# Kernel tuning notes

Hardware: AMD Instinct MI355X
Metric: run time of the kernel (lower is better)

Reference implementation:

```python
import jax, jax.numpy as jnp
import numpy as np

KERNEL_MUL = 2.0
KERNEL_NUM = 5


def setup_inputs() -> dict:
    key = jax.random.key(0)
    k1, k2 = jax.random.split(key)
    N, D = 4096, 512
    source = jax.random.normal(k1, (N, D), dtype=jnp.float32)
    target = jax.random.normal(k2, (N, D), dtype=jnp.float32)
    return {"source": source, "target": target}


def _mmd(source, target):
    n = source.shape[0]
    total = jnp.concatenate([source, target], axis=0)  # [2N, D]
    # pairwise squared L2 via the ||a||^2 + ||b||^2 - 2 a.b identity (same math,
    # avoids materializing the [2N,2N,D] expanded tensor the torch code builds)
    sq = jnp.sum(total * total, axis=1)  # [2N]
    L2 = sq[:, None] + sq[None, :] - 2.0 * (total @ total.T)  # [2N, 2N]
    m = total.shape[0]
    # torch uses L2_distance.data -> detached bandwidth
    bandwidth = jax.lax.stop_gradient(jnp.sum(L2)) / (m * m - m)
    bandwidth = bandwidth / (KERNEL_MUL ** (KERNEL_NUM // 2))
    kernels = jnp.zeros_like(L2)
    for i in range(KERNEL_NUM):
        kernels = kernels + jnp.exp(-L2 / (bandwidth * (KERNEL_MUL ** i)))
    XX = kernels[:n, :n]
    YY = kernels[n:, n:]
    XY = kernels[:n, n:]
    YX = kernels[n:, :n]
    return jnp.mean(XX + YY - XY - YX)


def reference(source, target):
    return _mmd(source, target)
```

## Files before the change

### kernel.cpp

```cpp
#include <hip/hip_runtime.h>
#include <hip/hip_fp8.h>

#define NHALF 4096
#define NROWS 8192
#define D 512
#define BM 128
#define BKB 128
#define NKT (D / BKB)
#define NB (NROWS / BM)
#define NTRI (NB * (NB + 1) / 2)

typedef float f32x4 __attribute__((ext_vector_type(4)));

__device__ __forceinline__ const float* row_ptr(const float* __restrict__ src,
                                                const float* __restrict__ tgt, int r) {
    return (r < NHALF) ? (src + (size_t)r * D) : (tgt + (size_t)(r - NHALF) * D);
}

__global__ __launch_bounds__(256)
void conv_stats(const float* __restrict__ src, const float* __restrict__ tgt,
                unsigned char* __restrict__ tot8, float* __restrict__ sq,
                float* __restrict__ colsum, double* __restrict__ sumsq) {
    __shared__ float cs_lds[4][512];
    int t = threadIdx.x, l = t & 63, w = t >> 6;
    int rbase = blockIdx.x * 64 + w * 16;

    float cs[8] = {0.f, 0.f, 0.f, 0.f, 0.f, 0.f, 0.f, 0.f};
    float ssq = 0.f;

    for (int rr = 0; rr < 16; ++rr) {
        int r = rbase + rr;
        const float* p = row_ptr(src, tgt, r) + l * 8;
        float4 v0 = *(const float4*)p;
        float4 v1 = *(const float4*)(p + 4);
        union { unsigned long long u; unsigned char b[8]; } q;
        q.b[0] = __hip_fp8_e4m3(v0.x).__x; q.b[1] = __hip_fp8_e4m3(v0.y).__x;
        q.b[2] = __hip_fp8_e4m3(v0.z).__x; q.b[3] = __hip_fp8_e4m3(v0.w).__x;
        q.b[4] = __hip_fp8_e4m3(v1.x).__x; q.b[5] = __hip_fp8_e4m3(v1.y).__x;
        q.b[6] = __hip_fp8_e4m3(v1.z).__x; q.b[7] = __hip_fp8_e4m3(v1.w).__x;
        unsigned dstu = (unsigned)((l & 48) | ((l & 15) ^ (r & 15)));
        *(unsigned long long*)&tot8[(size_t)r * D + dstu * 8] = q.u;

        float s8 = v0.x*v0.x + v0.y*v0.y + v0.z*v0.z + v0.w*v0.w
                 + v1.x*v1.x + v1.y*v1.y + v1.z*v1.z + v1.w*v1.w;
        ssq += s8;
        cs[0] += v0.x; cs[1] += v0.y; cs[2] += v0.z; cs[3] += v0.w;
        cs[4] += v1.x; cs[5] += v1.y; cs[6] += v1.z; cs[7] += v1.w;
        float rsum = s8;
        for (int off = 32; off > 0; off >>= 1) rsum += __shfl_down(rsum, off);
        if (l == 0) sq[r] = rsum;
    }
#pragma unroll
    for (int j = 0; j < 8; ++j) cs_lds[w][l * 8 + j] = cs[j];
    for (int off = 32; off > 0; off >>= 1) ssq += __shfl_down(ssq, off);
    __shared__ float wssq[4];
    if (l == 0) wssq[w] = ssq;
    __syncthreads();
    int c0 = t * 2;
    float a = cs_lds[0][c0] + cs_lds[1][c0] + cs_lds[2][c0] + cs_lds[3][c0];
    float b = cs_lds[0][c0+1] + cs_lds[1][c0+1] + cs_lds[2][c0+1] + cs_lds[3][c0+1];
    atomicAdd(&colsum[c0], a);
    atomicAdd(&colsum[c0 + 1], b);
    if (t == 0) atomicAdd(sumsq, (double)(wssq[0] + wssq[1] + wssq[2] + wssq[3]));
}

__global__ void bw_kernel(const float* __restrict__ colsum, const double* __restrict__ sumsq,
                          float* __restrict__ inv16bw) {
    __shared__ double red[512];
    int c = threadIdx.x;
    double v = (double)colsum[c];
    red[c] = v * v;
    __syncthreads();
    for (int s = 256; s > 0; s >>= 1) {
        if (c < s) red[c] += red[c + s];
        __syncthreads();
    }
    if (c == 0) {
        double m = (double)NROWS;
        double sumL2 = 2.0 * m * sumsq[0] - 2.0 * red[0];
        double bw = sumL2 / (m * m - m);
        bw = bw / 4.0;
        inv16bw[0] = (float)(1.0 / (16.0 * bw));
    }
}

__global__ __launch_bounds__(256)
void mmd_main(const unsigned char* __restrict__ tot8,
              const float* __restrict__ sq, const float* __restrict__ inv16bw_p,
              double* __restrict__ S) {
    int b = blockIdx.x;
    int ti = (b & 7) * (NTRI / 8) + (b >> 3);
    int bi = (int)(64.5f - sqrtf(64.5f * 64.5f - 2.0f * (float)ti));
    if (bi < 0) bi = 0;
    while (bi > 0 && bi * NB - bi * (bi - 1) / 2 > ti) --bi;
    while ((bi + 1) * NB - (bi + 1) * bi / 2 <= ti) ++bi;
    int bj = bi + (ti - (bi * NB - bi * (bi - 1) / 2));

    __shared__ __align__(16) unsigned char As[BM * BKB];
    __shared__ __align__(16) unsigned char Bs[BM * BKB];

    int t = threadIdx.x, l = t & 63, w = t >> 6;
    int wr = w >> 1, wc = w & 1;
    int m = l & 15, kg = l >> 4;

    const unsigned char* ab = tot8 + (size_t)(bi * BM) * D;
    const unsigned char* bb = tot8 + (size_t)(bj * BM) * D;

    f32x4 acc[4][4];
#pragma unroll
    for (int i = 0; i < 4; ++i)
#pragma unroll
        for (int j = 0; j < 4; ++j)
            acc[i][j] = (f32x4){0.f, 0.f, 0.f, 0.f};

    for (int kt = 0; kt < NKT; ++kt) {
        __syncthreads();
#pragma unroll
        for (int i = 0; i < 4; ++i) {
            int g = i * 256 + t;
            int row = g >> 3, ch = g & 7;
            __builtin_amdgcn_global_load_lds(
                (const __attribute__((address_space(1))) void*)(ab + (size_t)row * D + kt * BKB + ch * 16),
                (__attribute__((address_space(3))) void*)(As + g * 16),
                16, 0, 0);
            __builtin_amdgcn_global_load_lds(
                (const __attribute__((address_space(1))) void*)(bb + (size_t)row * D + kt * BKB + ch * 16),
                (__attribute__((address_space(3))) void*)(Bs + g * 16),
                16, 0, 0);
        }
        __syncthreads();

#pragma unroll
        for (int ks = 0; ks < 4; ++ks) {
            long af[4], bfr[4];
#pragma unroll
            for (int fi = 0; fi < 4; ++fi) {
                int row = wr * 64 + fi * 16 + m;
                int unit = (ks * 4 + kg) ^ m;
                af[fi] = *(const long*)&As[row * BKB + unit * 8];
            }
#pragma unroll
            for (int fj = 0; fj < 4; ++fj) {
                int row = wc * 64 + fj * 16 + m;
                int unit = (ks * 4 + kg) ^ m;
                bfr[fj] = *(const long*)&Bs[row * BKB + unit * 8];
            }
#pragma unroll
            for (int fi = 0; fi < 4; ++fi)
#pragma unroll
                for (int fj = 0; fj < 4; ++fj)
                    acc[fi][fj] = __builtin_amdgcn_mfma_f32_16x16x32_fp8_fp8(af[fi], bfr[fj], acc[fi][fj], 0, 0, 0);
        }
    }

    float inv16bw = inv16bw_p[0];
    float coef = ((bi == bj) ? 1.f : 2.f) * (((bi < NB / 2) == (bj < NB / 2)) ? 1.f : -1.f);

    float sqj[4];
#pragma unroll
    for (int fj = 0; fj < 4; ++fj) sqj[fj] = sq[bj * BM + wc * 64 + fj * 16 + m];
    int ib = bi * BM + wr * 64 + kg * 4;

    float local = 0.f;
#pragma unroll
    for (int fi = 0; fi < 4; ++fi) {
        float sqi[4];
#pragma unroll
        for (int j = 0; j < 4; ++j) sqi[j] = sq[ib + fi * 16 + j];
#pragma unroll
        for (int fj = 0; fj < 4; ++fj) {
#pragma unroll
            for (int j = 0; j < 4; ++j) {
                float L2 = sqi[j] + sqj[fj] - 2.f * acc[fi][fj][j];
                float u = __expf(-L2 * inv16bw);
                float ks = u;
                u *= u; ks += u;
                u *= u; ks += u;
                u *= u; ks += u;
                u *= u; ks += u;
                if (bi == bj) {
                    int ig = wr * 64 + fi * 16 + kg * 4 + j;
                    int jg = wc * 64 + fj * 16 + m;
                    if (ig == jg) ks = 5.0f;
                }
                local += ks;
            }
        }
    }
    local *= coef;

    for (int off = 32; off > 0; off >>= 1) local += __shfl_down(local, off);
    __shared__ float wsum[4];
    if ((t & 63) == 0) wsum[t >> 6] = local;
    __syncthreads();
    if (t == 0) {
        float bsum = wsum[0] + wsum[1] + wsum[2] + wsum[3];
        atomicAdd(S, (double)bsum);
    }
}

__global__ void finalize_kernel(const double* __restrict__ S, float* __restrict__ out) {
    out[0] = (float)(S[0] / ((double)NHALF * (double)NHALF));
}

extern "C" void kernel_launch(void* const* d_in, const int* in_sizes, int n_in,
                              void* d_out, int out_size, void* d_ws, size_t ws_size,
                              hipStream_t stream) {
    const float* src = (const float*)d_in[0];
    const float* tgt = (const float*)d_in[1];
    float* out = (float*)d_out;
    char* ws = (char*)d_ws;

    unsigned char* tot8 = (unsigned char*)ws;
    float*  sq      = (float*)(ws + 4194304);
    float*  colsum  = (float*)(ws + 4194304 + 32768);
    double* sumsq   = (double*)(ws + 4194304 + 34816);
    double* S       = (double*)(ws + 4194304 + 34824);
    float*  inv16bw = (float*)(ws + 4194304 + 34832);

    hipMemsetAsync(ws + 4194304 + 32768, 0, 2068, stream);

    conv_stats<<<128, 256, 0, stream>>>(src, tgt, tot8, sq, colsum, sumsq);
    bw_kernel<<<1, 512, 0, stream>>>(colsum, sumsq, inv16bw);
    mmd_main<<<NTRI, 256, 0, stream>>>(tot8, sq, inv16bw, S);
    finalize_kernel<<<1, 1, 0, stream>>>(S, out);
}
```

Before: 73.73 us.

## Use scaled 16x16x128 fp8 MFMA, fold bandwidth calc into main kernel

Replaces four 16x16x32 fp8 MFMAs per fragment with one gfx950 scaled 16x16x128 f8f6f4 MFMA, using unit scales. This cuts the MFMA instruction count, and the LDS fragment reads are regrouped per k-tile. The separate bandwidth kernel is removed: every main block recomputes inv16bw from colsum while its first tile loads, which saves a launch but repeats a small reduction in each block (in float instead of double). conv_stats also gets twice as many blocks with half the rows each, and mmd_main gets a launch-bounds occupancy hint of 3.

```diff
diff --git a/kernel.cpp b/kernel.cpp
--- a/kernel.cpp
+++ b/kernel.cpp
@@ -11,6 +11,7 @@
 #define NTRI (NB * (NB + 1) / 2)
 
 typedef float f32x4 __attribute__((ext_vector_type(4)));
+typedef int   v8i   __attribute__((ext_vector_type(8)));
 
 __device__ __forceinline__ const float* row_ptr(const float* __restrict__ src,
                                                 const float* __restrict__ tgt, int r) {
@@ -23,12 +24,12 @@
                 float* __restrict__ colsum, double* __restrict__ sumsq) {
     __shared__ float cs_lds[4][512];
     int t = threadIdx.x, l = t & 63, w = t >> 6;
-    int rbase = blockIdx.x * 64 + w * 16;
+    int rbase = blockIdx.x * 32 + w * 8;
 
     float cs[8] = {0.f, 0.f, 0.f, 0.f, 0.f, 0.f, 0.f, 0.f};
     float ssq = 0.f;
 
-    for (int rr = 0; rr < 16; ++rr) {
+    for (int rr = 0; rr < 8; ++rr) {
         int r = rbase + rr;
         const float* p = row_ptr(src, tgt, r) + l * 8;
         float4 v0 = *(const float4*)p;
@@ -64,30 +65,10 @@
     if (t == 0) atomicAdd(sumsq, (double)(wssq[0] + wssq[1] + wssq[2] + wssq[3]));
 }
 
-__global__ void bw_kernel(const float* __restrict__ colsum, const double* __restrict__ sumsq,
-                          float* __restrict__ inv16bw) {
-    __shared__ double red[512];
-    int c = threadIdx.x;
-    double v = (double)colsum[c];
-    red[c] = v * v;
-    __syncthreads();
-    for (int s = 256; s > 0; s >>= 1) {
-        if (c < s) red[c] += red[c + s];
-        __syncthreads();
-    }
-    if (c == 0) {
-        double m = (double)NROWS;
-        double sumL2 = 2.0 * m * sumsq[0] - 2.0 * red[0];
-        double bw = sumL2 / (m * m - m);
-        bw = bw / 4.0;
-        inv16bw[0] = (float)(1.0 / (16.0 * bw));
-    }
-}
-
-__global__ __launch_bounds__(256)
+__global__ __launch_bounds__(256, 3)
 void mmd_main(const unsigned char* __restrict__ tot8,
-              const float* __restrict__ sq, const float* __restrict__ inv16bw_p,
-              double* __restrict__ S) {
+              const float* __restrict__ sq, const float* __restrict__ colsum,
+              const double* __restrict__ sumsq, double* __restrict__ S) {
     int b = blockIdx.x;
     int ti = (b & 7) * (NTRI / 8) + (b >> 3);
     int bi = (int)(64.5f - sqrtf(64.5f * 64.5f - 2.0f * (float)ti));
@@ -106,15 +87,7 @@
     const unsigned char* ab = tot8 + (size_t)(bi * BM) * D;
     const unsigned char* bb = tot8 + (size_t)(bj * BM) * D;
 
-    f32x4 acc[4][4];
-#pragma unroll
-    for (int i = 0; i < 4; ++i)
-#pragma unroll
-        for (int j = 0; j < 4; ++j)
-            acc[i][j] = (f32x4){0.f, 0.f, 0.f, 0.f};
-
-    for (int kt = 0; kt < NKT; ++kt) {
-        __syncthreads();
+    auto stage = [&](int kt) {
 #pragma unroll
         for (int i = 0; i < 4; ++i) {
             int g = i * 256 + t;
@@ -128,32 +101,65 @@
                 (__attribute__((address_space(3))) void*)(Bs + g * 16),
                 16, 0, 0);
         }
-        __syncthreads();
-
-#pragma unroll
-        for (int ks = 0; ks < 4; ++ks) {
-            long af[4], bfr[4];
-#pragma unroll
-            for (int fi = 0; fi < 4; ++fi) {
-                int row = wr * 64 + fi * 16 + m;
-                int unit = (ks * 4 + kg) ^ m;
-                af[fi] = *(const long*)&As[row * BKB + unit * 8];
+    };
+
+    stage(0);
+
+    float c1 = colsum[t], c2 = colsum[t + 256];
+    float part = c1 * c1 + c2 * c2;
+    for (int off = 32; off > 0; off >>= 1) part += __shfl_down(part, off);
+    __shared__ float bwl[4];
+    if (l == 0) bwl[w] = part;
+    __syncthreads();
+    float sumcol2 = bwl[0] + bwl[1] + bwl[2] + bwl[3];
+    double md = (double)NROWS;
+    double sumL2 = 2.0 * md * sumsq[0] - 2.0 * (double)sumcol2;
+    double bwv = sumL2 / (md * md - md) / 4.0;
+    float inv16bw = (float)(1.0 / (16.0 * bwv));
+
+    f32x4 acc[4][4];
+#pragma unroll
+    for (int i = 0; i < 4; ++i)
+#pragma unroll
+        for (int j = 0; j < 4; ++j)
+            acc[i][j] = (f32x4){0.f, 0.f, 0.f, 0.f};
+
+    __syncthreads();
+
+    for (int kt = 0; kt < NKT; ++kt) {
+        union Frag { v8i v; long q[4]; };
+        Frag fa[4];
+#pragma unroll
+        for (int fi = 0; fi < 4; ++fi) {
+            int row = wr * 64 + fi * 16 + m;
+#pragma unroll
+            for (int q = 0; q < 4; ++q) {
+                int unit = (q * 4 + kg) ^ m;
+                fa[fi].q[q] = *(const long*)&As[row * BKB + unit * 8];
             }
-#pragma unroll
-            for (int fj = 0; fj < 4; ++fj) {
-                int row = wc * 64 + fj * 16 + m;
-                int unit = (ks * 4 + kg) ^ m;
-                bfr[fj] = *(const long*)&Bs[row * BKB + unit * 8];
+        }
+#pragma unroll
+        for (int fj = 0; fj < 4; ++fj) {
+            Frag fb;
+            int row = wc * 64 + fj * 16 + m;
+#pragma unroll
+            for (int q = 0; q < 4; ++q) {
+                int unit = (q * 4 + kg) ^ m;
+                fb.q[q] = *(const long*)&Bs[row * BKB + unit * 8];
             }
 #pragma unroll
             for (int fi = 0; fi < 4; ++fi)
-#pragma unroll
-                for (int fj = 0; fj < 4; ++fj)
-                    acc[fi][fj] = __builtin_amdgcn_mfma_f32_16x16x32_fp8_fp8(af[fi], bfr[fj], acc[fi][fj], 0, 0, 0);
-        }
-    }
-
-    float inv16bw = inv16bw_p[0];
+                acc[fi][fj] = __builtin_amdgcn_mfma_scale_f32_16x16x128_f8f6f4(
+                    fa[fi].v, fb.v, acc[fi][fj], 0, 0,
+                    0, 0x7F7F7F7F, 0, 0x7F7F7F7F);
+        }
+        if (kt + 1 < NKT) {
+            __syncthreads();
+            stage(kt + 1);
+            __syncthreads();
+        }
+    }
+
     float coef = ((bi == bj) ? 1.f : 2.f) * (((bi < NB / 2) == (bj < NB / 2)) ? 1.f : -1.f);
 
     float sqj[4];
@@ -216,12 +222,10 @@
     float*  colsum  = (float*)(ws + 4194304 + 32768);
     double* sumsq   = (double*)(ws + 4194304 + 34816);
     double* S       = (double*)(ws + 4194304 + 34824);
-    float*  inv16bw = (float*)(ws + 4194304 + 34832);
-
-    hipMemsetAsync(ws + 4194304 + 32768, 0, 2068, stream);
-
-    conv_stats<<<128, 256, 0, stream>>>(src, tgt, tot8, sq, colsum, sumsq);
-    bw_kernel<<<1, 512, 0, stream>>>(colsum, sumsq, inv16bw);
-    mmd_main<<<NTRI, 256, 0, stream>>>(tot8, sq, inv16bw, S);
+
+    hipMemsetAsync(ws + 4194304 + 32768, 0, 2064, stream);
+
+    conv_stats<<<256, 256, 0, stream>>>(src, tgt, tot8, sq, colsum, sumsq);
+    mmd_main<<<NTRI, 256, 0, stream>>>(tot8, sq, colsum, sumsq, S);
     finalize_kernel<<<1, 1, 0, stream>>>(S, out);
 }
```

Result: no change. 73.13 us (-0.8%).

## Fuse bandwidth reduction into conv kernel and use 8-wave GEMM blocks

Applied to the files above, without the earlier changes.

The separate bandwidth kernel is folded into conv_stats: the last block to finish, found with an atomic ticket, reduces the column sums and writes the inverse bandwidth, which removes one kernel launch. conv_stats now uses twice as many blocks with half the rows each. mmd_main moves to 512 threads and 8 waves per 128x128 tile, so each wave computes a 64x32 sub-tile, giving fewer accumulator registers and more waves to hide latency. The trade is more per-tile syncs and fewer MFMAs per wave between them, and the memset still covers the ticket, so the fused path stays correct.

```diff
diff --git a/kernel.cpp b/kernel.cpp
--- a/kernel.cpp
+++ b/kernel.cpp
@@ -9,6 +9,7 @@
 #define NKT (D / BKB)
 #define NB (NROWS / BM)
 #define NTRI (NB * (NB + 1) / 2)
+#define CONV_BLOCKS 256
 
 typedef float f32x4 __attribute__((ext_vector_type(4)));
 
@@ -20,15 +21,19 @@
 __global__ __launch_bounds__(256)
 void conv_stats(const float* __restrict__ src, const float* __restrict__ tgt,
                 unsigned char* __restrict__ tot8, float* __restrict__ sq,
-                float* __restrict__ colsum, double* __restrict__ sumsq) {
+                float* __restrict__ colsum, double* __restrict__ sumsq,
+                unsigned* __restrict__ ticket, float* __restrict__ inv16bw_out) {
     __shared__ float cs_lds[4][512];
+    __shared__ float wssq[4];
+    __shared__ int lastFlag;
+    __shared__ double red[256];
     int t = threadIdx.x, l = t & 63, w = t >> 6;
-    int rbase = blockIdx.x * 64 + w * 16;
+    int rbase = blockIdx.x * 32 + w * 8;
 
     float cs[8] = {0.f, 0.f, 0.f, 0.f, 0.f, 0.f, 0.f, 0.f};
     float ssq = 0.f;
 
-    for (int rr = 0; rr < 16; ++rr) {
+    for (int rr = 0; rr < 8; ++rr) {
         int r = rbase + rr;
         const float* p = row_ptr(src, tgt, r) + l * 8;
         float4 v0 = *(const float4*)p;
@@ -53,7 +58,6 @@
 #pragma unroll
     for (int j = 0; j < 8; ++j) cs_lds[w][l * 8 + j] = cs[j];
     for (int off = 32; off > 0; off >>= 1) ssq += __shfl_down(ssq, off);
-    __shared__ float wssq[4];
     if (l == 0) wssq[w] = ssq;
     __syncthreads();
     int c0 = t * 2;
@@ -62,29 +66,34 @@
     atomicAdd(&colsum[c0], a);
     atomicAdd(&colsum[c0 + 1], b);
     if (t == 0) atomicAdd(sumsq, (double)(wssq[0] + wssq[1] + wssq[2] + wssq[3]));
-}
-
-__global__ void bw_kernel(const float* __restrict__ colsum, const double* __restrict__ sumsq,
-                          float* __restrict__ inv16bw) {
-    __shared__ double red[512];
-    int c = threadIdx.x;
-    double v = (double)colsum[c];
-    red[c] = v * v;
-    __syncthreads();
-    for (int s = 256; s > 0; s >>= 1) {
-        if (c < s) red[c] += red[c + s];
+    __syncthreads();
+
+    if (t == 0) {
+        __threadfence();
+        unsigned old = atomicAdd(ticket, 1u);
+        lastFlag = (old == CONV_BLOCKS - 1) ? 1 : 0;
+    }
+    __syncthreads();
+    if (lastFlag) {
+        float ca = atomicAdd(&colsum[t], 0.f);
+        float cb = atomicAdd(&colsum[t + 256], 0.f);
+        red[t] = (double)ca * ca + (double)cb * cb;
         __syncthreads();
-    }
-    if (c == 0) {
-        double m = (double)NROWS;
-        double sumL2 = 2.0 * m * sumsq[0] - 2.0 * red[0];
-        double bw = sumL2 / (m * m - m);
-        bw = bw / 4.0;
-        inv16bw[0] = (float)(1.0 / (16.0 * bw));
-    }
-}
-
-__global__ __launch_bounds__(256)
+        for (int s = 128; s > 0; s >>= 1) {
+            if (t < s) red[t] += red[t + s];
+            __syncthreads();
+        }
+        if (t == 0) {
+            double ssqd = atomicAdd(sumsq, 0.0);
+            double m = (double)NROWS;
+            double sumL2 = 2.0 * m * ssqd - 2.0 * red[0];
+            double bw = sumL2 / (m * m - m) / 4.0;
+            inv16bw_out[0] = (float)(1.0 / (16.0 * bw));
+        }
+    }
+}
+
+__global__ __launch_bounds__(512, 4)
 void mmd_main(const unsigned char* __restrict__ tot8,
               const float* __restrict__ sq, const float* __restrict__ inv16bw_p,
               double* __restrict__ S) {
@@ -100,24 +109,24 @@
     __shared__ __align__(16) unsigned char Bs[BM * BKB];
 
     int t = threadIdx.x, l = t & 63, w = t >> 6;
-    int wr = w >> 1, wc = w & 1;
+    int wr = w >> 2, wc = w & 3;
     int m = l & 15, kg = l >> 4;
 
     const unsigned char* ab = tot8 + (size_t)(bi * BM) * D;
     const unsigned char* bb = tot8 + (size_t)(bj * BM) * D;
 
-    f32x4 acc[4][4];
+    f32x4 acc[4][2];
 #pragma unroll
     for (int i = 0; i < 4; ++i)
 #pragma unroll
-        for (int j = 0; j < 4; ++j)
+        for (int j = 0; j < 2; ++j)
             acc[i][j] = (f32x4){0.f, 0.f, 0.f, 0.f};
 
     for (int kt = 0; kt < NKT; ++kt) {
         __syncthreads();
 #pragma unroll
-        for (int i = 0; i < 4; ++i) {
-            int g = i * 256 + t;
+        for (int i = 0; i < 2; ++i) {
+            int g = i * 512 + t;
             int row = g >> 3, ch = g & 7;
             __builtin_amdgcn_global_load_lds(
                 (const __attribute__((address_space(1))) void*)(ab + (size_t)row * D + kt * BKB + ch * 16),
@@ -132,7 +141,7 @@
 
 #pragma unroll
         for (int ks = 0; ks < 4; ++ks) {
-            long af[4], bfr[4];
+            long af[4], bfr[2];
 #pragma unroll
             for (int fi = 0; fi < 4; ++fi) {
                 int row = wr * 64 + fi * 16 + m;
@@ -140,15 +149,15 @@
                 af[fi] = *(const long*)&As[row * BKB + unit * 8];
             }
 #pragma unroll
-            for (int fj = 0; fj < 4; ++fj) {
-                int row = wc * 64 + fj * 16 + m;
+            for (int fj = 0; fj < 2; ++fj) {
+                int row = wc * 32 + fj * 16 + m;
                 int unit = (ks * 4 + kg) ^ m;
                 bfr[fj] = *(const long*)&Bs[row * BKB + unit * 8];
             }
 #pragma unroll
             for (int fi = 0; fi < 4; ++fi)
 #pragma unroll
-                for (int fj = 0; fj < 4; ++fj)
+                for (int fj = 0; fj < 2; ++fj)
                     acc[fi][fj] = __builtin_amdgcn_mfma_f32_16x16x32_fp8_fp8(af[fi], bfr[fj], acc[fi][fj], 0, 0, 0);
         }
     }
@@ -156,9 +165,9 @@
     float inv16bw = inv16bw_p[0];
     float coef = ((bi == bj) ? 1.f : 2.f) * (((bi < NB / 2) == (bj < NB / 2)) ? 1.f : -1.f);
 
-    float sqj[4];
-#pragma unroll
-    for (int fj = 0; fj < 4; ++fj) sqj[fj] = sq[bj * BM + wc * 64 + fj * 16 + m];
+    float sqj[2];
+#pragma unroll
+    for (int fj = 0; fj < 2; ++fj) sqj[fj] = sq[bj * BM + wc * 32 + fj * 16 + m];
     int ib = bi * BM + wr * 64 + kg * 4;
 
     float local = 0.f;
@@ -168,7 +177,7 @@
 #pragma unroll
         for (int j = 0; j < 4; ++j) sqi[j] = sq[ib + fi * 16 + j];
 #pragma unroll
-        for (int fj = 0; fj < 4; ++fj) {
+        for (int fj = 0; fj < 2; ++fj) {
 #pragma unroll
             for (int j = 0; j < 4; ++j) {
                 float L2 = sqi[j] + sqj[fj] - 2.f * acc[fi][fj][j];
@@ -180,7 +189,7 @@
                 u *= u; ks += u;
                 if (bi == bj) {
                     int ig = wr * 64 + fi * 16 + kg * 4 + j;
-                    int jg = wc * 64 + fj * 16 + m;
+                    int jg = wc * 32 + fj * 16 + m;
                     if (ig == jg) ks = 5.0f;
                 }
                 local += ks;
@@ -190,11 +199,12 @@
     local *= coef;
 
     for (int off = 32; off > 0; off >>= 1) local += __shfl_down(local, off);
-    __shared__ float wsum[4];
-    if ((t & 63) == 0) wsum[t >> 6] = local;
+    __shared__ float wsum[8];
+    if (l == 0) wsum[w] = local;
     __syncthreads();
     if (t == 0) {
-        float bsum = wsum[0] + wsum[1] + wsum[2] + wsum[3];
+        float bsum = wsum[0] + wsum[1] + wsum[2] + wsum[3]
+                   + wsum[4] + wsum[5] + wsum[6] + wsum[7];
         atomicAdd(S, (double)bsum);
     }
 }
@@ -212,16 +222,16 @@
     char* ws = (char*)d_ws;
 
     unsigned char* tot8 = (unsigned char*)ws;
-    float*  sq      = (float*)(ws + 4194304);
-    float*  colsum  = (float*)(ws + 4194304 + 32768);
-    double* sumsq   = (double*)(ws + 4194304 + 34816);
-    double* S       = (double*)(ws + 4194304 + 34824);
-    float*  inv16bw = (float*)(ws + 4194304 + 34832);
+    float*    sq      = (float*)(ws + 4194304);
+    float*    colsum  = (float*)(ws + 4194304 + 32768);
+    double*   sumsq   = (double*)(ws + 4194304 + 34816);
+    double*   S       = (double*)(ws + 4194304 + 34824);
+    unsigned* ticket  = (unsigned*)(ws + 4194304 + 34832);
+    float*    inv16bw = (float*)(ws + 4194304 + 34836);
 
     hipMemsetAsync(ws + 4194304 + 32768, 0, 2068, stream);
 
-    conv_stats<<<128, 256, 0, stream>>>(src, tgt, tot8, sq, colsum, sumsq);
-    bw_kernel<<<1, 512, 0, stream>>>(colsum, sumsq, inv16bw);
-    mmd_main<<<NTRI, 256, 0, stream>>>(tot8, sq, inv16bw, S);
+    conv_stats<<<CONV_BLOCKS, 256, 0, stream>>>(src, tgt, tot8, sq, colsum, sumsq, ticket, inv16bw);
+    mmd_main<<<NTRI, 512, 0, stream>>>(tot8, sq, inv16bw, S);
     finalize_kernel<<<1, 1, 0, stream>>>(S, out);
 }
```

Measured after the change: 74.02 us. No clear change (+0.4%).
